# Optimization experiments

Hardware: AMD Instinct MI355X
Metric: run time of the kernel (lower is better)

## Reference

```python
import jax, jax.numpy as jnp
import numpy as np

NUM_LAYERS = 3
INPUT_SIZE = 64
EMB = 128
NUM_CAT = 128          # must equal EMB for the W_e_proj assignment to shape-check
NUM_QUERIES = 1
INIT_SCALE = 0.02
KERNEL_PARAM = 1.0     # referenced-but-undefined in source; standard alpha=1
B = 16
N = 2048
D = INPUT_SIZE + 2 * EMB                 # 320, transformer embedding dim
F_IN = INPUT_SIZE + NUM_CAT + EMB        # 320, raw input feature dim


def setup_inputs() -> dict:
    key = jax.random.key(0)
    k = jax.random.split(key, 6)
    x = jax.random.normal(k[0], (B, F_IN, N), dtype=jnp.float32)
    embedding_matrix = jax.random.normal(k[1], (EMB, NUM_CAT), dtype=jnp.float32)
    W_Q = jax.random.normal(k[2], (NUM_LAYERS, 1, D, D), dtype=jnp.float32) * INIT_SCALE
    W_K = jax.random.normal(k[3], (NUM_LAYERS, 1, D, D), dtype=jnp.float32) * INIT_SCALE
    W_V = jax.random.normal(k[4], (NUM_LAYERS, 1, D, D), dtype=jnp.float32) * INIT_SCALE
    P = jax.random.normal(k[5], (NUM_LAYERS, 1, D, D), dtype=jnp.float32) * INIT_SCALE
    return {"x": x, "embedding_matrix": embedding_matrix,
            "W_Q": W_Q, "W_K": W_K, "W_V": W_V, "P": P}


def _build_We(embedding_matrix):
    W = jnp.zeros((D, F_IN), dtype=embedding_matrix.dtype)
    W = W.at[:INPUT_SIZE, :INPUT_SIZE].set(jnp.eye(INPUT_SIZE, dtype=W.dtype))
    W = W.at[D - EMB:, F_IN - EMB:].set(jnp.eye(EMB, dtype=W.dtype))
    # rows [input_size : D-emb], cols [input_size : F-num_categories]
    W = W.at[INPUT_SIZE:D - EMB, INPUT_SIZE:F_IN - NUM_CAT].set(embedding_matrix)
    return W


def reference(x, embedding_matrix, W_Q, W_K, W_V, P):
    W = _build_We(embedding_matrix)
    h = jnp.einsum('df,bfn->bdn', W, x)                        # [B, D, N]
    for nl in range(NUM_LAYERS):
        key = h[:, :, :-NUM_QUERIES]                           # include_query=False
        value = key
        query = h
        n_context = key.shape[-1]
        Q = jnp.einsum('id,bdm->bim', W_Q[nl, 0], query)       # [B, D, N]
        K = jnp.einsum('id,bdn->bin', W_K[nl, 0], key)         # [B, D, M]
        V = jnp.einsum('id,bdn->bin', W_V[nl, 0], value)       # [B, D, M]
        # linear kernel scores
        scores = KERNEL_PARAM * jnp.einsum('bim,bin->bmn', Q, K)  # [B, N, M]
        attn = jnp.einsum('bin,bmn->bim', V, scores) / n_context  # [B, D, N]
        h = h + jnp.einsum('ji,bim->bjm', P[nl, 0], attn)
    f = h[:, -EMB:, :]                                         # [B, EMB, N] (squeeze no-op for B>1)
    logits = jnp.einsum('bdn,dc->bnc', f, embedding_matrix)    # [B, N, C]
    predictions = jax.nn.softmax(logits, axis=-1)
    return logits, predictions
```

## Files before the change

kernel.cpp:

```cpp
#include <hip/hip_runtime.h>
#include <math.h>

typedef long long ll;
typedef unsigned int uint;
typedef unsigned short ushort;
typedef __attribute__((ext_vector_type(4))) float f32x4;
typedef __attribute__((ext_vector_type(8))) short bf16x8;

#define SZ 102400LL
#define RS 40960LL

__device__ inline void split2(float v, ushort& h, ushort& l)
{
    uint u = __float_as_uint(v);
    uint uh = u + (0x7FFFu + ((u >> 16) & 1u));
    h = (ushort)(uh >> 16);
    float hf = __uint_as_float((uint)h << 16);
    float d = v - hf;
    uint ud = __float_as_uint(d);
    l = (ushort)((ud + (0x7FFFu + ((ud >> 16) & 1u))) >> 16);
}
__device__ inline float us2f(ushort h, ushort l)
{
    return __uint_as_float((uint)h << 16) + __uint_as_float((uint)l << 16);
}

__global__ __launch_bounds__(256) void gram_sp_k(
    const float* __restrict__ x, float* __restrict__ part,
    const float* __restrict__ Wq, const float* __restrict__ Wk,
    const float* __restrict__ Wv, const float* __restrict__ P,
    const float* __restrict__ emb,
    ushort* __restrict__ WqTs, ushort* __restrict__ WkTs, ushort* __restrict__ WvTs,
    ushort* __restrict__ Ps, ushort* __restrict__ embs, ushort* __restrict__ embTs,
    float* __restrict__ q0)
{
    __shared__ __align__(16) char smem[20480];
    int bid0 = blockIdx.x, tid = threadIdx.x;
    if (bid0 < 960) {
        ushort* Ah  = (ushort*)smem;
        ushort* Al_ = Ah + 2560;
        ushort* Bh  = Al_ + 2560;
        ushort* Bl_ = Bh + 2560;
        int flat = bid0;
        int swz = (flat & 7) * 120 + (flat >> 3);
        int b = swz / 60;
        int rr = swz - b * 60;
        int p = rr / 15, t = rr - p * 15;
        int ti = 0, rem = t;
        while (rem >= 5 - ti) { rem -= 5 - ti; ++ti; }
        int tj = ti + rem;
        int i0 = ti * 64, j0 = tj * 64;
        bool diag = (ti == tj);
        const float* X = x + (ll)b * 320 * 2048;
        int wv = tid >> 6, lane = tid & 63;
        int lr = lane & 15, kb = (lane >> 4) * 8;
        int cr = tid >> 2, ck = (tid & 3) * 8;
        f32x4 hh[4], hl[4], lh[4];
        f32x4 zz = {0.f, 0.f, 0.f, 0.f};
        #pragma unroll
        for (int f = 0; f < 4; ++f) { hh[f] = zz; hl[f] = zz; lh[f] = zz; }
        const ushort* BhS = diag ? Ah : Bh;
        const ushort* BlS = diag ? Al_ : Bl_;

        for (int it = 0; it < 16; ++it) {
            int kg0 = p * 512 + it * 32;
            {
                const float* src = X + (ll)(i0 + cr) * 2048 + kg0 + ck;
                float4 v0 = *(const float4*)src;
                float4 v1 = *(const float4*)(src + 4);
                float vals[8] = {v0.x,v0.y,v0.z,v0.w,v1.x,v1.y,v1.z,v1.w};
                if (kg0 + ck + 7 >= 2047) {
                    #pragma unroll
                    for (int u = 0; u < 8; ++u) if (kg0 + ck + u >= 2047) vals[u] = 0.f;
                }
                bf16x8 hv, lv;
                #pragma unroll
                for (int u = 0; u < 8; ++u) { ushort h, l; split2(vals[u], h, l);
                                              hv[u] = (short)h; lv[u] = (short)l; }
                *(bf16x8*)&Ah[cr * 40 + ck] = hv;
                *(bf16x8*)&Al_[cr * 40 + ck] = lv;
            }
            if (!diag) {
                const float* src = X + (ll)(j0 + cr) * 2048 + kg0 + ck;
                float4 v0 = *(const float4*)src;
                float4 v1 = *(const float4*)(src + 4);
                float vals[8] = {v0.x,v0.y,v0.z,v0.w,v1.x,v1.y,v1.z,v1.w};
                if (kg0 + ck + 7 >= 2047) {
                    #pragma unroll
                    for (int u = 0; u < 8; ++u) if (kg0 + ck + u >= 2047) vals[u] = 0.f;
                }
                bf16x8 hv, lv;
                #pragma unroll
                for (int u = 0; u < 8; ++u) { ushort h, l; split2(vals[u], h, l);
                                              hv[u] = (short)h; lv[u] = (short)l; }
                *(bf16x8*)&Bh[cr * 40 + ck] = hv;
                *(bf16x8*)&Bl_[cr * 40 + ck] = lv;
            }
            __syncthreads();
            bf16x8 ah = *(const bf16x8*)&Ah[(wv * 16 + lr) * 40 + kb];
            bf16x8 al = *(const bf16x8*)&Al_[(wv * 16 + lr) * 40 + kb];
            #pragma unroll
            for (int f = 0; f < 4; ++f) {
                bf16x8 bh_ = *(const bf16x8*)&BhS[(f * 16 + lr) * 40 + kb];
                bf16x8 bl_ = *(const bf16x8*)&BlS[(f * 16 + lr) * 40 + kb];
                hh[f] = __builtin_amdgcn_mfma_f32_16x16x32_bf16(ah, bh_, hh[f], 0, 0, 0);
                hl[f] = __builtin_amdgcn_mfma_f32_16x16x32_bf16(ah, bl_, hl[f], 0, 0, 0);
                lh[f] = __builtin_amdgcn_mfma_f32_16x16x32_bf16(al, bh_, lh[f], 0, 0, 0);
            }
            __syncthreads();
        }
        float* out = part + (((ll)p * 16 + b) * 15 + t) * 4096;
        int orow0 = wv * 16 + (lane >> 4) * 4;
        #pragma unroll
        for (int f = 0; f < 4; ++f) {
            int col = f * 16 + lr;
            #pragma unroll
            for (int r = 0; r < 4; ++r)
                out[(orow0 + r) * 64 + col] = hh[f][r] + hl[f][r] + lh[f][r];
        }
        return;
    }
    int bid = bid0 - 960;
    float (*T)[65] = (float(*)[65])smem;
    if (bid < 225) {
        int m = bid / 25, t = bid % 25;
        const float* mats[3] = {Wq, Wk, Wv};
        ushort* dsts[3] = {WqTs, WkTs, WvTs};
        const float* src = mats[m / 3] + (ll)(m % 3) * SZ;
        ushort* dst = dsts[m / 3] + (ll)(m % 3) * SZ;
        int r0 = (t / 5) * 64, c0 = (t % 5) * 64;
        #pragma unroll
        for (int s = 0; s < 4; ++s) {
            int idx = s * 256 + tid;
            int r = idx >> 4, cq = (idx & 15) * 4;
            *(float4*)&T[r][cq] = *(const float4*)(src + (ll)(r0 + r) * 320 + c0 + cq);
        }
        __syncthreads();
        {
            int c = tid >> 2, kq = (tid & 3) * 16;
            bf16x8 h0, h1, l0, l1;
            #pragma unroll
            for (int u = 0; u < 8; ++u) {
                ushort h, l;
                split2(T[kq + u][c], h, l);     h0[u] = (short)h; l0[u] = (short)l;
                split2(T[kq + 8 + u][c], h, l); h1[u] = (short)h; l1[u] = (short)l;
            }
            ushort* dh = dst + (ll)(c0 + c) * 320 + r0 + kq;
            *(bf16x8*)dh = h0; *(bf16x8*)(dh + 8) = h1;
            *(bf16x8*)(dh + 3 * SZ) = l0; *(bf16x8*)(dh + 3 * SZ + 8) = l1;
        }
    } else if (bid < 375) {
        ll off = (ll)(bid - 225) * 2048 + tid * 8;
        float4 v0 = *(const float4*)(P + off);
        float4 v1 = *(const float4*)(P + off + 4);
        float vals[8] = {v0.x,v0.y,v0.z,v0.w,v1.x,v1.y,v1.z,v1.w};
        bf16x8 hv, lv;
        #pragma unroll
        for (int u = 0; u < 8; ++u) { ushort h,l; split2(vals[u],h,l);
                                      hv[u]=(short)h; lv[u]=(short)l; }
        *(bf16x8*)(Ps + off) = hv;
        *(bf16x8*)(Ps + off + 3 * SZ) = lv;
    } else if (bid < 383) {
        ll off = (ll)(bid - 375) * 2048 + tid * 8;
        float4 v0 = *(const float4*)(emb + off);
        float4 v1 = *(const float4*)(emb + off + 4);
        float vals[8] = {v0.x,v0.y,v0.z,v0.w,v1.x,v1.y,v1.z,v1.w};
        bf16x8 hv, lv;
        #pragma unroll
        for (int u = 0; u < 8; ++u) { ushort h,l; split2(vals[u],h,l);
                                      hv[u]=(short)h; lv[u]=(short)l; }
        *(bf16x8*)(embs + off) = hv;
        *(bf16x8*)(embs + off + 16384) = lv;
    } else if (bid < 387) {
        int t = bid - 383;
        int r0 = (t >> 1) * 64, c0 = (t & 1) * 64;
        {
            int r = tid >> 2, cq = (tid & 3) * 4;
            *(float4*)&T[r][cq]      = *(const float4*)(emb + (ll)(r0 + r) * 128 + c0 + cq);
            *(float4*)&T[r][cq + 16] = *(const float4*)(emb + (ll)(r0 + r) * 128 + c0 + cq + 16);
            *(float4*)&T[r][cq + 32] = *(const float4*)(emb + (ll)(r0 + r) * 128 + c0 + cq + 32);
            *(float4*)&T[r][cq + 48] = *(const float4*)(emb + (ll)(r0 + r) * 128 + c0 + cq + 48);
        }
        __syncthreads();
        {
            int c = tid >> 2, kq = (tid & 3) * 16;
            bf16x8 h0, h1, l0, l1;
            #pragma unroll
            for (int u = 0; u < 8; ++u) {
                ushort h, l;
                split2(T[kq + u][c], h, l);     h0[u]=(short)h; l0[u]=(short)l;
                split2(T[kq + 8 + u][c], h, l); h1[u]=(short)h; l1[u]=(short)l;
            }
            ushort* dh = embTs + (ll)(c0 + c) * 128 + r0 + kq;
            *(bf16x8*)dh = h0; *(bf16x8*)(dh + 8) = h1;
            *(bf16x8*)(dh + 16384) = l0; *(bf16x8*)(dh + 16384 + 8) = l1;
        }
    } else {
        ll base = (ll)(bid - 387) * 2048;
        #pragma unroll
        for (int s = 0; s < 8; ++s) {
            ll id = base + s * 256 + tid;
            int c = (int)(id / 320), i = (int)(id % 320);
            q0[id] = (i >= 192) ? emb[(ll)(i - 192) * 128 + c] : 0.f;
        }
    }
}

__global__ __launch_bounds__(256) void gram_red_k(const float* __restrict__ part,
                                                  ushort* __restrict__ GxS,
                                                  ushort* __restrict__ T1s)
{
    int bt = blockIdx.x;
    int b = bt / 15, t = bt % 15;
    int ti = 0, rem = t;
    while (rem >= 5 - ti) { rem -= 5 - ti; ++ti; }
    int tj = ti + rem;
    int i0 = ti * 64, j0 = tj * 64;
    int tid = threadIdx.x;
    int tx = tid & 15, rg = tid >> 4;
    bool wi = (ti == 0 || ti >= 3);
    bool wj = (tj == 0 || tj >= 3);
    ushort* Gb = GxS + (ll)b * SZ;
    ushort* Tsb = T1s + (ll)b * SZ;
    #pragma unroll
    for (int m = 0; m < 4; ++m) {
        int r = rg * 4 + m;
        float s[4] = {};
        for (int p = 0; p < 4; ++p) {
            const float* src = part + (((ll)p * 16 + b) * 15 + t) * 4096 + r * 64 + tx * 4;
            float4 v = *(const float4*)src;
            s[0]+=v.x; s[1]+=v.y; s[2]+=v.z; s[3]+=v.w;
        }
        #pragma unroll
        for (int u = 0; u < 4; ++u) {
            ushort h, l; split2(s[u], h, l);
            ll rd = (ll)(i0 + r) * 320 + j0 + tx * 4 + u;
            ll rt = (ll)(j0 + tx * 4 + u) * 320 + (i0 + r);
            Gb[rd] = h; Gb[rd + 16 * SZ] = l;
            Gb[rt] = h; Gb[rt + 16 * SZ] = l;
            if (wi) { Tsb[rd] = h; Tsb[rd + 16 * SZ] = l; }
            if (wj) { Tsb[rt] = h; Tsb[rt + 16 * SZ] = l; }
        }
    }
}

struct CJob {
    const ushort *Ah, *Bh;
    const void *Ci, *Ci2;
    float* C; ushort* Cs;
    ll aB, bB, ciB, ci2B, cB, csB;
    ll aLo, bLo, csLo, ciLo, ci2Lo;
    int aS, bS, ciS, ci2S, cS, csS;
    int K, tN, tpb, flags;
    int swzQ, swzR;
    float alpha;
};
struct CPack { CJob j[4]; };

__global__ __launch_bounds__(256) void mchain_k(CPack jp, int c0, int c1, int c2)
{
    int bid = blockIdx.x;
    int ji, local;
    if (bid < c0)      { ji = 0; local = bid; }
    else if (bid < c1) { ji = 1; local = bid - c0; }
    else if (bid < c2) { ji = 2; local = bid - c1; }
    else               { ji = 3; local = bid - c2; }
    CJob j = jp.j[ji];
    int xcd = local & 7, sidx = local >> 3;
    int base = (xcd < j.swzR) ? xcd * (j.swzQ + 1)
                              : j.swzR * (j.swzQ + 1) + (xcd - j.swzR) * j.swzQ;
    int swz = base + sidx;
    int bz = swz / j.tpb;
    int t = swz - bz * j.tpb;
    int i0 = (t / j.tN) * 64, j0 = (t % j.tN) * 64;
    int tid = threadIdx.x;
    int wv = tid >> 6, lane = tid & 63;
    int lr = lane & 15, kb = (lane >> 4) * 8;
    f32x4 hh[4], cx[4];
    f32x4 zz = {0.f,0.f,0.f,0.f};
    #pragma unroll
    for (int f = 0; f < 4; ++f) { hh[f] = zz; cx[f] = zz; }

    __shared__ __align__(16) ushort Bsh[2][2][2560];

    if (j.K > 0) {
        int srow = tid >> 2, skq = (tid & 3) * 8;
        const ushort* Bg = j.Bh + (ll)bz * j.bB + (ll)(j0 + srow) * j.bS + skq;
        const ushort* Ar = j.Ah + (ll)bz * j.aB + (ll)(i0 + wv * 16 + lr) * j.aS + kb;
        bf16x8 svh, svl, ah, al, ahn, aln;
        svh = *(const bf16x8*)Bg;
        svl = *(const bf16x8*)(Bg + j.bLo);
        *(bf16x8*)&Bsh[0][0][srow * 40 + skq] = svh;
        *(bf16x8*)&Bsh[0][1][srow * 40 + skq] = svl;
        ah = *(const bf16x8*)Ar;
        al = *(const bf16x8*)(Ar + j.aLo);
        __syncthreads();
        int nit = j.K >> 5;
        for (int it = 0; it < nit; ++it) {
            int cur = it & 1;
            bool more = (it + 1 < nit);
            if (more) {
                int k1 = (it + 1) << 5;
                svh = *(const bf16x8*)(Bg + k1);
                svl = *(const bf16x8*)(Bg + j.bLo + k1);
                ahn = *(const bf16x8*)(Ar + k1);
                aln = *(const bf16x8*)(Ar + j.aLo + k1);
            }
            #pragma unroll
            for (int f = 0; f < 4; ++f) {
                bf16x8 bh = *(const bf16x8*)&Bsh[cur][0][(f * 16 + lr) * 40 + kb];
                bf16x8 bl = *(const bf16x8*)&Bsh[cur][1][(f * 16 + lr) * 40 + kb];
                hh[f] = __builtin_amdgcn_mfma_f32_16x16x32_bf16(ah, bh, hh[f], 0, 0, 0);
                cx[f] = __builtin_amdgcn_mfma_f32_16x16x32_bf16(ah, bl, cx[f], 0, 0, 0);
                cx[f] = __builtin_amdgcn_mfma_f32_16x16x32_bf16(al, bh, cx[f], 0, 0, 0);
            }
            if (more) {
                *(bf16x8*)&Bsh[cur ^ 1][0][srow * 40 + skq] = svh;
                *(bf16x8*)&Bsh[cur ^ 1][1][srow * 40 + skq] = svl;
                ah = ahn; al = aln;
            }
            __syncthreads();
        }
    }
    const float* Cif = (const float*)j.Ci;
    const ushort* Ciu = (const ushort*)j.Ci;
    const float* Ci2f = (const float*)j.Ci2;
    const ushort* Ci2u = (const ushort*)j.Ci2;
    float* Cp = j.C + (ll)bz * j.cB;
    ushort* Csp = j.Cs + (ll)bz * j.csB;
    int r0 = i0 + wv * 16 + ((lane >> 4) << 2);
    #pragma unroll
    for (int f = 0; f < 4; ++f) {
        int col = j0 + f * 16 + lr;
        #pragma unroll
        for (int r = 0; r < 4; ++r) {
            int row = r0 + r;
            float v = j.alpha * (hh[f][r] + cx[f][r]);
            if (j.flags & 1)
                v += Cif[(ll)bz * j.ciB + (ll)row * j.ciS + col];
            if (j.flags & 32) {
                const ushort* p = Ciu + (ll)bz * j.ciB + (ll)row * j.ciS + col;
                v += us2f(p[0], p[j.ciLo]);
            }
            if (j.flags & 64) {
                const ushort* b2 = Ci2u + (ll)bz * j.ci2B;
                if (j.flags & 2) { const ushort* p = b2 + (ll)row * j.ci2S + col;
                                   v += us2f(p[0], p[j.ci2Lo]); }
                if (j.flags & 4) { const ushort* p = b2 + (ll)col * j.ci2S + row;
                                   v += us2f(p[0], p[j.ci2Lo]); }
            } else {
                if (j.flags & 2) v += Ci2f[(ll)bz * j.ci2B + (ll)row * j.ci2S + col];
                if (j.flags & 4) v += Ci2f[(ll)bz * j.ci2B + (ll)col * j.ci2S + row];
            }
            if (j.flags & 8) Cp[(ll)row * j.cS + col] = v;
            if (j.flags & 16) {
                ushort h, l; split2(v, h, l);
                ushort* p = Csp + (ll)row * j.csS + col;
                p[0] = h; p[j.csLo] = l;
            }
        }
    }
}

__global__ __launch_bounds__(256) void logits_mfma_k(const float* __restrict__ x,
                                                     const ushort* __restrict__ LBs,
                                                     float* __restrict__ logits,
                                                     float* __restrict__ pred)
{
    int flat = blockIdx.x;
    int swzb = (flat & 7) * 128 + (flat >> 3);
    int b = swzb >> 6;
    int i0 = (swzb & 63) * 32;
    const float* X = x + (ll)b * 320 * 2048;
    const ushort* LB = LBs + (ll)b * RS;
    __shared__ float Xs_[2][32][33];
    __shared__ float SB[32][132];
    __shared__ float pmL[2][32], psL[2][32];
    int tid = threadIdx.x;
    int wv = tid >> 6, lane = tid & 63;
    int lr = lane & 15, g = lane >> 4, kb = g * 8;
    int rowg = (wv & 1) * 16, ch = wv >> 1, colh = ch * 64;
    int lkk = tid >> 3, lq = (tid & 7) * 4;
    f32x4 hh[4], cx[4];
    f32x4 zz = {0.f,0.f,0.f,0.f};
    #pragma unroll
    for (int f = 0; f < 4; ++f) { hh[f] = zz; cx[f] = zz; }
    float4 pa;
    auto glb = [&](int k0) {
        pa = *(const float4*)(X + (ll)(k0 + lkk) * 2048 + i0 + lq);
    };
    auto stl = [&](int buf) {
        float* p = &Xs_[buf][lkk][lq];
        p[0] = pa.x; p[1] = pa.y; p[2] = pa.z; p[3] = pa.w;
    };
    glb(0); stl(0);
    __syncthreads();
    for (int it = 0; it < 10; ++it) {
        int cur = it & 1;
        if (it < 9) glb((it + 1) * 32);
        const ushort* B0 = LB + (ll)(colh + lr) * 320 + it * 32 + kb;
        bf16x8 b0h = *(const bf16x8*)B0;
        bf16x8 b0l = *(const bf16x8*)(B0 + 16 * RS);
        bf16x8 b1h = *(const bf16x8*)(B0 + 16 * 320);
        bf16x8 b1l = *(const bf16x8*)(B0 + 16 * 320 + 16 * RS);
        bf16x8 b2h = *(const bf16x8*)(B0 + 32 * 320);
        bf16x8 b2l = *(const bf16x8*)(B0 + 32 * 320 + 16 * RS);
        bf16x8 b3h = *(const bf16x8*)(B0 + 48 * 320);
        bf16x8 b3l = *(const bf16x8*)(B0 + 48 * 320 + 16 * RS);
        bf16x8 ah, al;
        #pragma unroll
        for (int u = 0; u < 8; ++u) {
            ushort h, l;
            split2(Xs_[cur][kb + u][rowg + lr], h, l);
            ah[u] = (short)h; al[u] = (short)l;
        }
        hh[0] = __builtin_amdgcn_mfma_f32_16x16x32_bf16(ah, b0h, hh[0], 0, 0, 0);
        cx[0] = __builtin_amdgcn_mfma_f32_16x16x32_bf16(ah, b0l, cx[0], 0, 0, 0);
        cx[0] = __builtin_amdgcn_mfma_f32_16x16x32_bf16(al, b0h, cx[0], 0, 0, 0);
        hh[1] = __builtin_amdgcn_mfma_f32_16x16x32_bf16(ah, b1h, hh[1], 0, 0, 0);
        cx[1] = __builtin_amdgcn_mfma_f32_16x16x32_bf16(ah, b1l, cx[1], 0, 0, 0);
        cx[1] = __builtin_amdgcn_mfma_f32_16x16x32_bf16(al, b1h, cx[1], 0, 0, 0);
        hh[2] = __builtin_amdgcn_mfma_f32_16x16x32_bf16(ah, b2h, hh[2], 0, 0, 0);
        cx[2] = __builtin_amdgcn_mfma_f32_16x16x32_bf16(ah, b2l, cx[2], 0, 0, 0);
        cx[2] = __builtin_amdgcn_mfma_f32_16x16x32_bf16(al, b2h, cx[2], 0, 0, 0);
        hh[3] = __builtin_amdgcn_mfma_f32_16x16x32_bf16(ah, b3h, hh[3], 0, 0, 0);
        cx[3] = __builtin_amdgcn_mfma_f32_16x16x32_bf16(ah, b3l, cx[3], 0, 0, 0);
        cx[3] = __builtin_amdgcn_mfma_f32_16x16x32_bf16(al, b3h, cx[3], 0, 0, 0);
        if (it < 9) stl(cur ^ 1);
        __syncthreads();
    }
    float v[4][4];
    #pragma unroll
    for (int r = 0; r < 4; ++r)
        #pragma unroll
        for (int f = 0; f < 4; ++f) v[r][f] = hh[f][r] + cx[f][r];
    #pragma unroll
    for (int r = 0; r < 4; ++r) {
        float m = fmaxf(fmaxf(v[r][0], v[r][1]), fmaxf(v[r][2], v[r][3]));
        #pragma unroll
        for (int off = 8; off; off >>= 1) m = fmaxf(m, __shfl_xor(m, off));
        if (lr == 0) pmL[ch][rowg + g * 4 + r] = m;
    }
    __syncthreads();
    float ev[4][4], inv[4];
    #pragma unroll
    for (int r = 0; r < 4; ++r) {
        int blr = rowg + g * 4 + r;
        float mx = fmaxf(pmL[0][blr], pmL[1][blr]);
        float s = 0.f;
        #pragma unroll
        for (int f = 0; f < 4; ++f) { ev[r][f] = expf(v[r][f] - mx); s += ev[r][f]; }
        #pragma unroll
        for (int off = 8; off; off >>= 1) s += __shfl_xor(s, off);
        if (lr == 0) psL[ch][blr] = s;
    }
    __syncthreads();
    #pragma unroll
    for (int r = 0; r < 4; ++r) {
        int blr = rowg + g * 4 + r;
        inv[r] = 1.f / (psL[0][blr] + psL[1][blr]);
    }
    #pragma unroll
    for (int r = 0; r < 4; ++r)
        #pragma unroll
        for (int f = 0; f < 4; ++f)
            SB[rowg + g * 4 + r][colh + f * 16 + lr] = v[r][f];
    __syncthreads();
    #pragma unroll
    for (int s = 0; s < 4; ++s) {
        int idx = s * 256 + tid;
        int row = idx >> 5, cq = (idx & 31) * 4;
        *(float4*)(logits + ((ll)b * 2048 + i0 + row) * 128 + cq) = *(float4*)&SB[row][cq];
    }
    __syncthreads();
    #pragma unroll
    for (int r = 0; r < 4; ++r)
        #pragma unroll
        for (int f = 0; f < 4; ++f)
            SB[rowg + g * 4 + r][colh + f * 16 + lr] = ev[r][f] * inv[r];
    __syncthreads();
    #pragma unroll
    for (int s = 0; s < 4; ++s) {
        int idx = s * 256 + tid;
        int row = idx >> 5, cq = (idx & 31) * 4;
        *(float4*)(pred + ((ll)b * 2048 + i0 + row) * 128 + cq) = *(float4*)&SB[row][cq];
    }
}

extern "C" void kernel_launch(void* const* d_in, const int* in_sizes, int n_in,
                              void* d_out, int out_size, void* d_ws, size_t ws_size,
                              hipStream_t stream)
{
    const float* x   = (const float*)d_in[0];
    const float* emb = (const float*)d_in[1];
    const float* Wq  = (const float*)d_in[2];
    const float* Wk  = (const float*)d_in[3];
    const float* Wv  = (const float*)d_in[4];
    const float* P   = (const float*)d_in[5];

    float* logits = (float*)d_out;
    float* pred   = logits + (ll)16 * 2048 * 128;

    float* w = (float*)d_ws;
    auto takef = [&](ll n) { float* p = w; w += n; return p; };
    ushort* GxS  = (ushort*)takef(16 * SZ);
    ushort* T1s  = (ushort*)takef(16 * SZ);
    ushort* Gs   = (ushort*)takef(16 * SZ);
    ushort* As   = (ushort*)takef(16 * SZ);
    ushort* Us   = (ushort*)takef(16 * SZ);
    float*  ATsF = takef(48 * SZ);
    ushort* ATs  = (ushort*)ATsF;
    ushort* PVs  = (ushort*)takef(3 * SZ);
    ushort* KQTs = (ushort*)takef(3 * SZ);
    ushort* KQs  = (ushort*)takef(3 * SZ);
    ushort* Ps   = (ushort*)takef(3 * SZ);
    ushort* WqTs = (ushort*)takef(3 * SZ);
    ushort* WkTs = (ushort*)takef(3 * SZ);
    ushort* WvTs = (ushort*)takef(3 * SZ);
    ushort* embs = (ushort*)takef(16384);
    ushort* embTs= (ushort*)takef(16384);
    float*  q0f  = takef(RS);
    ushort* q1s  = (ushort*)takef(16 * RS);
    ushort* q2s  = (ushort*)takef(16 * RS);
    ushort* LBs  = (ushort*)takef(16 * RS);
    ushort* Xs   = GxS;
    ushort* Zts  = T1s;
    float*  part = ATsF;
    ushort* q3s  = q1s;
    const float cinv = 1.f / 2047.f;

    auto JB = [](const ushort* Ah, ll aB, int aS, ll aLo,
                 const ushort* Bh, ll bB, int bS, ll bLo,
                 int K, int tM, int tN, float alpha, int flags,
                 const void* Ci, ll ciB, int ciS, ll ciLo,
                 const void* Ci2, ll ci2B, int ci2S, ll ci2Lo,
                 float* C, ll cB, int cS,
                 ushort* Cs, ll csB, int csS, ll csLo) {
        CJob j;
        j.Ah = Ah; j.Bh = Bh;
        j.Ci = Ci; j.Ci2 = Ci2; j.C = C; j.Cs = Cs;
        j.aB = aB; j.bB = bB; j.ciB = ciB; j.ci2B = ci2B; j.cB = cB; j.csB = csB;
        j.aLo = aLo; j.bLo = bLo; j.csLo = csLo; j.ciLo = ciLo; j.ci2Lo = ci2Lo;
        j.aS = aS; j.bS = bS; j.ciS = ciS; j.ci2S = ci2S; j.cS = cS; j.csS = csS;
        j.K = K; j.tN = tN; j.tpb = tM * tN; j.flags = flags; j.alpha = alpha;
        j.swzQ = 0; j.swzR = 0;
        return j;
    };
    auto fire = [&](const CJob* js, const int* nb, int n) {
        CPack jp;
        int cum[4], tot = 0;
        for (int i = 0; i < 4; ++i) {
            jp.j[i] = js[i < n ? i : 0];
            if (i < n) { jp.j[i].swzQ = nb[i] >> 3; jp.j[i].swzR = nb[i] & 7; }
            tot += (i < n ? nb[i] : 0);
            cum[i] = tot;
        }
        mchain_k<<<tot, 256, 0, stream>>>(jp, cum[0], cum[1], cum[2]);
    };

    gram_sp_k<<<1367, 256, 0, stream>>>(x, part, Wq, Wk, Wv, P, emb,
                                        WqTs, WkTs, WvTs, Ps, embs, embTs, q0f);
    gram_red_k<<<240, 256, 0, stream>>>(part, GxS, T1s);
    {
        CJob js[4] = {
            JB(embs, 0, 128, 16384,  GxS + 64, SZ, 320, 16*SZ,  128, 2, 5, 1.f, 16,
               0,0,0,0, 0,0,0,0,  0,0,0,  T1s + 64*320, SZ, 320, 16*SZ),
            JB(Ps, SZ, 320, 3*SZ,  WvTs, SZ, 320, 3*SZ,  320, 5, 5, 1.f, 16,
               0,0,0,0, 0,0,0,0,  0,0,0,  PVs, SZ, 320, 3*SZ),
            JB(WqTs, SZ, 320, 3*SZ,  WkTs, SZ, 320, 3*SZ,  320, 5, 5, 1.f, 16,
               0,0,0,0, 0,0,0,0,  0,0,0,  KQTs, SZ, 320, 3*SZ),
            JB(WkTs, SZ, 320, 3*SZ,  WqTs, SZ, 320, 3*SZ,  320, 5, 5, 1.f, 16,
               0,0,0,0, 0,0,0,0,  0,0,0,  KQs, SZ, 320, 3*SZ)};
        int nb[4] = {160, 75, 75, 75};
        fire(js, nb, 4);
    }
    {
        CJob js[3] = {
            JB(T1s + 64, SZ, 320, 16*SZ,  embs, 0, 128, 16384,  128, 5, 2, 1.f, 16,
               0,0,0,0, 0,0,0,0,  0,0,0,  Gs + 64, SZ, 320, 16*SZ),
            JB(0,0,0,0, 0,0,0,0,  0, 5, 1, 0.f, 32|16,
               T1s, SZ, 320, 16*SZ, 0,0,0,0,  0,0,0,  Gs, SZ, 320, 16*SZ),
            JB(0,0,0,0, 0,0,0,0,  0, 5, 2, 0.f, 32|16,
               T1s + 192, SZ, 320, 16*SZ, 0,0,0,0,  0,0,0,  Gs + 192, SZ, 320, 16*SZ)};
        int nb[3] = {160, 80, 160};
        fire(js, nb, 3);
    }
    for (int l = 0; l < 3; ++l) {
        const ushort* PVl = PVs + (ll)l * SZ;
        const ushort* KQTl = KQTs + (ll)l * SZ;
        const ushort* KQl = KQs + (ll)l * SZ;
        ushort* ATl = ATs + (ll)l * 16 * SZ;
        if (l < 2) {
            CJob s1[2] = {
                JB(PVl, 0, 320, 3*SZ,  Gs, SZ, 320, 16*SZ,  320, 5, 5, 1.f, 16,
                   0,0,0,0, 0,0,0,0,  0,0,0,  Xs, SZ, 320, 16*SZ),
                JB(Gs, SZ, 320, 16*SZ,  KQl, 0, 320, 3*SZ,  320, 5, 5, 1.f, 16,
                   0,0,0,0, 0,0,0,0,  0,0,0,  Zts, SZ, 320, 16*SZ)};
            int n1[2] = {400, 400};
            fire(s1, n1, 2);
            CJob s2[3] = {
                JB(Xs, SZ, 320, 16*SZ,  KQTl, 0, 320, 3*SZ,  320, 5, 5, cinv, 16,
                   0,0,0,0, 0,0,0,0,  0,0,0,  As, SZ, 320, 16*SZ),
                JB(KQTl, 0, 320, 3*SZ,  Xs, SZ, 320, 16*SZ,  320, 5, 5, cinv, 16,
                   0,0,0,0, 0,0,0,0,  0,0,0,  ATl, SZ, 320, 48*SZ),
                JB(Xs, SZ, 320, 16*SZ,  Zts, SZ, 320, 16*SZ,  320, 5, 5, cinv, 16,
                   0,0,0,0, 0,0,0,0,  0,0,0,  Us, SZ, 320, 16*SZ)};
            int n2[3] = {400, 400, 400};
            fire(s2, n2, 3);
            CJob s3[1] = {
                JB(Us, SZ, 320, 16*SZ,  As, SZ, 320, 16*SZ,  320, 5, 5, 1.f, 16|32|2|4|64,
                   Gs, SZ, 320, 16*SZ,  Us, SZ, 320, 16*SZ,  0,0,0,  Gs, SZ, 320, 16*SZ)};
            int n3[1] = {400};
            fire(s3, n3, 1);
        } else {
            CJob s1[1] = {
                JB(PVl, 0, 320, 3*SZ,  Gs, SZ, 320, 16*SZ,  320, 5, 5, 1.f, 16,
                   0,0,0,0, 0,0,0,0,  0,0,0,  Xs, SZ, 320, 16*SZ)};
            int n1[1] = {400};
            fire(s1, n1, 1);
            CJob s2[1] = {
                JB(KQTl, 0, 320, 3*SZ,  Xs, SZ, 320, 16*SZ,  320, 5, 5, cinv, 16,
                   0,0,0,0, 0,0,0,0,  0,0,0,  ATl, SZ, 320, 48*SZ)};
            int n2[1] = {400};
            fire(s2, n2, 1);
        }
    }
    {
        CJob js[1] = {
            JB(embTs, 0, 128, 16384,  ATs + 2*16*SZ + 192, SZ, 320, 48*SZ,  128, 2, 5, 1.f, 1|16,
               q0f, 0, 320, 0, 0,0,0,0,  0,0,0,  q1s, RS, 320, 16*RS)};
        int nb[1] = {160};
        fire(js, nb, 1);
    }
    {
        CJob js[1] = {
            JB(q1s, RS, 320, 16*RS,  ATs + 1*16*SZ, SZ, 320, 48*SZ,  320, 2, 5, 1.f, 32|16,
               q1s, RS, 320, 16*RS, 0,0,0,0,  0,0,0,  q2s, RS, 320, 16*RS)};
        int nb[1] = {160};
        fire(js, nb, 1);
    }
    {
        CJob js[1] = {
            JB(q2s, RS, 320, 16*RS,  ATs, SZ, 320, 48*SZ,  320, 2, 5, 1.f, 32|16,
               q2s, RS, 320, 16*RS, 0,0,0,0,  0,0,0,  q3s, RS, 320, 16*RS)};
        int nb[1] = {160};
        fire(js, nb, 1);
    }
    {
        CJob js[3] = {
            JB(q3s + 64, RS, 320, 16*RS,  embTs, 0, 128, 16384,  128, 2, 2, 1.f, 16,
               0,0,0,0, 0,0,0,0,  0,0,0,  LBs + 64, RS, 320, 16*RS),
            JB(0,0,0,0, 0,0,0,0,  0, 2, 1, 0.f, 32|16,
               q3s, RS, 320, 16*RS, 0,0,0,0,  0,0,0,  LBs, RS, 320, 16*RS),
            JB(0,0,0,0, 0,0,0,0,  0, 2, 2, 0.f, 32|16,
               q3s + 192, RS, 320, 16*RS, 0,0,0,0,  0,0,0,  LBs + 192, RS, 320, 16*RS)};
        int nb[3] = {64, 32, 64};
        fire(js, nb, 3);
    }
    logits_mfma_k<<<1024, 256, 0, stream>>>(x, LBs, logits, pred);
}
```

Before: 315.9 us.

## Emit transposed bf16 x in gram kernel and use it for logits GEMM

The gram kernel's diagonal tiles already hold the bf16 high part of x in shared memory, so it now also writes a transposed [B,N,320] bf16 copy of x to workspace. A new logits kernel reads this pre-transposed copy directly into MFMA fragments instead of re-reading fp32 x and transposing through shared memory. This drops the low-part product for x (only hi·hi and hi·lo of the LB operand are kept), which trades some accuracy for fewer MFMAs and less traffic. The path is only taken when the workspace is large enough, and it adds extra global writes to the gram kernel.

New measurement: 320.8 us. About the same (+1.6%).

```diff
diff --git a/kernel.cpp b/kernel.cpp
--- a/kernel.cpp
+++ b/kernel.cpp
@@ -32,7 +32,7 @@
     const float* __restrict__ emb,
     ushort* __restrict__ WqTs, ushort* __restrict__ WkTs, ushort* __restrict__ WvTs,
     ushort* __restrict__ Ps, ushort* __restrict__ embs, ushort* __restrict__ embTs,
-    float* __restrict__ q0)
+    float* __restrict__ q0, ushort* __restrict__ xTh)
 {
     __shared__ __align__(16) char smem[20480];
     int bid0 = blockIdx.x, tid = threadIdx.x;
@@ -97,6 +97,22 @@
                 *(bf16x8*)&Bl_[cr * 40 + ck] = lv;
             }
             __syncthreads();
+            if (xTh && diag) {
+                int nl = tid >> 3, fq = (tid & 7) * 8;
+                int n = kg0 + nl;
+                bf16x8 v;
+                #pragma unroll
+                for (int u = 0; u < 8; ++u) v[u] = (short)Ah[(fq + u) * 40 + nl];
+                if (n == 2047) {
+                    #pragma unroll
+                    for (int u = 0; u < 8; ++u) {
+                        ushort h, l;
+                        split2(X[(ll)(i0 + fq + u) * 2048 + 2047], h, l);
+                        v[u] = (short)h;
+                    }
+                }
+                *(bf16x8*)&xTh[((ll)b * 2048 + n) * 320 + i0 + fq] = v;
+            }
             bf16x8 ah = *(const bf16x8*)&Ah[(wv * 16 + lr) * 40 + kb];
             bf16x8 al = *(const bf16x8*)&Al_[(wv * 16 + lr) * 40 + kb];
             #pragma unroll
@@ -362,6 +378,106 @@
     }
 }
 
+__global__ __launch_bounds__(256) void logits_v4_k(const ushort* __restrict__ xTh,
+                                                   const ushort* __restrict__ LBs,
+                                                   float* __restrict__ logits,
+                                                   float* __restrict__ pred)
+{
+    int flat = blockIdx.x;
+    int swzb = (flat & 7) * 128 + (flat >> 3);
+    int b = swzb >> 6;
+    int i0 = (swzb & 63) * 32;
+    const ushort* XT = xTh + (ll)b * 2048 * 320;
+    const ushort* LB = LBs + (ll)b * RS;
+    __shared__ float SB[32][132];
+    __shared__ float pmL[2][32], psL[2][32];
+    int tid = threadIdx.x;
+    int wv = tid >> 6, lane = tid & 63;
+    int lr = lane & 15, g = lane >> 4, kb = g * 8;
+    int rowg = (wv & 1) * 16, ch = wv >> 1, colh = ch * 64;
+    f32x4 hh[4], cx[4];
+    f32x4 zz = {0.f,0.f,0.f,0.f};
+    #pragma unroll
+    for (int f = 0; f < 4; ++f) { hh[f] = zz; cx[f] = zz; }
+    const ushort* Ar = XT + (ll)(i0 + rowg + lr) * 320 + kb;
+    for (int it = 0; it < 10; ++it) {
+        bf16x8 ah = *(const bf16x8*)(Ar + it * 32);
+        const ushort* B0 = LB + (ll)(colh + lr) * 320 + it * 32 + kb;
+        bf16x8 b0h = *(const bf16x8*)B0;
+        bf16x8 b0l = *(const bf16x8*)(B0 + 16 * RS);
+        bf16x8 b1h = *(const bf16x8*)(B0 + 16 * 320);
+        bf16x8 b1l = *(const bf16x8*)(B0 + 16 * 320 + 16 * RS);
+        bf16x8 b2h = *(const bf16x8*)(B0 + 32 * 320);
+        bf16x8 b2l = *(const bf16x8*)(B0 + 32 * 320 + 16 * RS);
+        bf16x8 b3h = *(const bf16x8*)(B0 + 48 * 320);
+        bf16x8 b3l = *(const bf16x8*)(B0 + 48 * 320 + 16 * RS);
+        hh[0] = __builtin_amdgcn_mfma_f32_16x16x32_bf16(ah, b0h, hh[0], 0, 0, 0);
+        cx[0] = __builtin_amdgcn_mfma_f32_16x16x32_bf16(ah, b0l, cx[0], 0, 0, 0);
+        hh[1] = __builtin_amdgcn_mfma_f32_16x16x32_bf16(ah, b1h, hh[1], 0, 0, 0);
+        cx[1] = __builtin_amdgcn_mfma_f32_16x16x32_bf16(ah, b1l, cx[1], 0, 0, 0);
+        hh[2] = __builtin_amdgcn_mfma_f32_16x16x32_bf16(ah, b2h, hh[2], 0, 0, 0);
+        cx[2] = __builtin_amdgcn_mfma_f32_16x16x32_bf16(ah, b2l, cx[2], 0, 0, 0);
+        hh[3] = __builtin_amdgcn_mfma_f32_16x16x32_bf16(ah, b3h, hh[3], 0, 0, 0);
+        cx[3] = __builtin_amdgcn_mfma_f32_16x16x32_bf16(ah, b3l, cx[3], 0, 0, 0);
+    }
+    float v[4][4];
+    #pragma unroll
+    for (int r = 0; r < 4; ++r)
+        #pragma unroll
+        for (int f = 0; f < 4; ++f) v[r][f] = hh[f][r] + cx[f][r];
+    #pragma unroll
+    for (int r = 0; r < 4; ++r) {
+        float m = fmaxf(fmaxf(v[r][0], v[r][1]), fmaxf(v[r][2], v[r][3]));
+        #pragma unroll
+        for (int off = 8; off; off >>= 1) m = fmaxf(m, __shfl_xor(m, off));
+        if (lr == 0) pmL[ch][rowg + g * 4 + r] = m;
+    }
+    __syncthreads();
+    float ev[4][4], inv[4];
+    #pragma unroll
+    for (int r = 0; r < 4; ++r) {
+        int blr = rowg + g * 4 + r;
+        float mx = fmaxf(pmL[0][blr], pmL[1][blr]);
+        float s = 0.f;
+        #pragma unroll
+        for (int f = 0; f < 4; ++f) { ev[r][f] = expf(v[r][f] - mx); s += ev[r][f]; }
+        #pragma unroll
+        for (int off = 8; off; off >>= 1) s += __shfl_xor(s, off);
+        if (lr == 0) psL[ch][blr] = s;
+    }
+    __syncthreads();
+    #pragma unroll
+    for (int r = 0; r < 4; ++r) {
+        int blr = rowg + g * 4 + r;
+        inv[r] = 1.f / (psL[0][blr] + psL[1][blr]);
+    }
+    #pragma unroll
+    for (int r = 0; r < 4; ++r)
+        #pragma unroll
+        for (int f = 0; f < 4; ++f)
+            SB[rowg + g * 4 + r][colh + f * 16 + lr] = v[r][f];
+    __syncthreads();
+    #pragma unroll
+    for (int s = 0; s < 4; ++s) {
+        int idx = s * 256 + tid;
+        int row = idx >> 5, cq = (idx & 31) * 4;
+        *(float4*)(logits + ((ll)b * 2048 + i0 + row) * 128 + cq) = *(float4*)&SB[row][cq];
+    }
+    __syncthreads();
+    #pragma unroll
+    for (int r = 0; r < 4; ++r)
+        #pragma unroll
+        for (int f = 0; f < 4; ++f)
+            SB[rowg + g * 4 + r][colh + f * 16 + lr] = ev[r][f] * inv[r];
+    __syncthreads();
+    #pragma unroll
+    for (int s = 0; s < 4; ++s) {
+        int idx = s * 256 + tid;
+        int row = idx >> 5, cq = (idx & 31) * 4;
+        *(float4*)(pred + ((ll)b * 2048 + i0 + row) * 128 + cq) = *(float4*)&SB[row][cq];
+    }
+}
+
 __global__ __launch_bounds__(256) void logits_mfma_k(const float* __restrict__ x,
                                                      const ushort* __restrict__ LBs,
                                                      float* __restrict__ logits,
@@ -523,6 +639,10 @@
     ushort* q1s  = (ushort*)takef(16 * RS);
     ushort* q2s  = (ushort*)takef(16 * RS);
     ushort* LBs  = (ushort*)takef(16 * RS);
+    ll base_floats = (ll)(w - (float*)d_ws);
+    ushort* xTh = nullptr;
+    if (ws_size >= (size_t)(base_floats + 5242880) * 4)
+        xTh = (ushort*)takef(5242880);
     ushort* Xs   = GxS;
     ushort* Zts  = T1s;
     float*  part = ATsF;
@@ -559,7 +679,7 @@
     };
 
     gram_sp_k<<<1367, 256, 0, stream>>>(x, part, Wq, Wk, Wv, P, emb,
-                                        WqTs, WkTs, WvTs, Ps, embs, embTs, q0f);
+                                        WqTs, WkTs, WvTs, Ps, embs, embTs, q0f, xTh);
     gram_red_k<<<240, 256, 0, stream>>>(part, GxS, T1s);
     {
         CJob js[4] = {
@@ -657,5 +777,8 @@
         int nb[3] = {64, 32, 64};
         fire(js, nb, 3);
     }
-    logits_mfma_k<<<1024, 256, 0, stream>>>(x, LBs, logits, pred);
+    if (xTh)
+        logits_v4_k<<<1024, 256, 0, stream>>>(xTh, LBs, logits, pred);
+    else
+        logits_mfma_k<<<1024, 256, 0, stream>>>(x, LBs, logits, pred);
 }
```
